# Optimization experiments

Hardware: AMD Instinct MI355X
Metric: run time of the kernel (lower is better)

The kernel has to match this reference:

```python
import jax, jax.numpy as jnp
import numpy as np

B, S, DIM = 2, 2048, 2048
H, KVH = 16, 8
HD = DIM // H            # 128
WIN = 512                # sliding window size
GLOB = 64                # global tokens
NEG = -1000000000.0


def _alibi_slopes(n):
    cp2 = 2.0 ** jnp.floor(jnp.log2(jnp.float32(n)))
    base = 2.0 ** (-(2.0 ** (-(jnp.log2(cp2) - 3.0))))
    powers = jnp.arange(1, 1 + n, dtype=jnp.float32)
    return jnp.power(base, powers)  # [n]


def _rope_tables(head_dim, seq_len, dtype=jnp.float32, base=10000.0):
    half = head_dim // 2
    freqs = 1.0 / base ** (jnp.arange(0, half, dtype=dtype) / half)
    t = jnp.arange(seq_len, dtype=dtype)
    f = jnp.outer(t, freqs)                       # [S, half]
    return jnp.sin(f)[None, None], jnp.cos(f)[None, None]  # [1,1,S,half]


def _rotary(x, sin, cos):
    # x: [b,h,s,d]; nonstandard rotation per source module
    x1, x2 = jnp.split(x, 2, axis=-1)
    return jnp.concatenate([x1 * cos - x2 * sin, x1 * sin + x2 * cos], axis=-1)


def _window_mask(seq_len):
    # Faithful to create_sliding_window_mask: 0.0 inside window / global rows+cols, -1e9 elsewhere
    i = jnp.arange(seq_len)[:, None]
    j = jnp.arange(seq_len)[None, :]
    m = jnp.where(jnp.abs(i - j) <= WIN // 2, 0.0, NEG)
    m = jnp.where((i < GLOB) | (j < GLOB), 0.0, m)
    return m  # [S, S] float


def setup_inputs() -> dict:
    key = jax.random.key(0)
    k1, k2, k3, k4 = jax.random.split(key, 4)
    x = jax.random.normal(k1, (B, S, DIM), dtype=jnp.float32)
    Wq = jax.random.normal(k2, (DIM, DIM), dtype=jnp.float32) * 0.02
    Wkv = jax.random.normal(k3, (DIM, 2 * KVH * HD), dtype=jnp.float32) * 0.02
    Wo = jax.random.normal(k4, (DIM, DIM), dtype=jnp.float32) * 0.02
    bo = jnp.zeros((DIM,), dtype=jnp.float32)
    return {"x": x, "Wq": Wq, "Wkv": Wkv, "Wo": Wo, "bo": bo}


def reference(x, Wq, Wkv, Wo, bo):
    b, s, dim = x.shape
    # token-complexity gating on queries
    complexity = jax.nn.sigmoid(jnp.sum(jnp.abs(x), axis=-1, keepdims=True))  # [b,s,1]
    q = jnp.dot(x * complexity, Wq)       # [b,s,dim]
    kv = jnp.dot(x, Wkv)                  # [b,s,2*kv_dim]
    k, v = jnp.split(kv, 2, axis=-1)

    q = q.reshape(b, s, H, HD).transpose(0, 2, 1, 3)      # [b,H,s,d]
    k = k.reshape(b, s, KVH, HD).transpose(0, 2, 1, 3)    # [b,KVH,s,d]
    v = v.reshape(b, s, KVH, HD).transpose(0, 2, 1, 3)

    sin, cos = _rope_tables(HD, s, dtype=x.dtype)
    q = _rotary(q, sin, cos)
    k = _rotary(k, sin, cos)

    r = H // KVH
    k = jnp.repeat(k, r, axis=1)   # 'b h s d -> b (h r) s d'
    v = jnp.repeat(v, r, axis=1)

    scale = 1.0 / jnp.sqrt(jnp.float32(HD)).astype(x.dtype)
    qk = jnp.einsum('bhid,bhjd->bhij', q, k) * scale      # [b,H,s,s]

    # ALiBi bias
    slopes = _alibi_slopes(H)                             # [H]
    pos = jnp.arange(s)
    dist = -jnp.abs(pos[:, None] - pos[None, :]).astype(jnp.float32)  # [s,s]
    qk = qk + slopes[:, None, None] * dist                # broadcast over batch

    # Faithful to source: jnp.where(float_mask, qk, NEG) treats nonzero (-1e9,
    # i.e. OUTSIDE window) as True -> keeps qk; zero (inside window) -> NEG.
    m = _window_mask(s)
    qk = jnp.where(m != 0.0, qk, NEG)

    attn = jax.nn.softmax(qk, axis=-1)
    out = jnp.einsum('bhij,bhjd->bhid', attn, v)          # [b,H,s,d]
    out = out.transpose(0, 2, 1, 3).reshape(b, s, dim)
    out = jnp.dot(out, Wo) + bo
    return out
```

## Files before the change

### kernel.cpp

```cpp
#include <hip/hip_runtime.h>

#define DEVI static __device__ __forceinline__

typedef __attribute__((ext_vector_type(8))) short short8;
typedef __attribute__((ext_vector_type(4))) short short4v;
typedef __attribute__((ext_vector_type(4))) float f32x4;

DEVI float bf2f(short u) {
  union { unsigned u32; float f; } c;
  c.u32 = ((unsigned)(unsigned short)u) << 16;
  return c.f;
}
DEVI short f2bf(float f) {
  union { float f; unsigned u32; } c; c.f = f;
  unsigned x = c.u32;
  unsigned r = (x + 0x7FFFu + ((x >> 16) & 1u)) >> 16;
  return (short)(unsigned short)r;
}
DEVI float ex2(float x) {
  float r;
  asm("v_exp_f32 %0, %1" : "=v"(r) : "v"(x));
  return r;
}
DEVI unsigned cvtpk(float lo, float hi) {
  unsigned r;
  asm("v_cvt_pk_bf16_f32 %0, %1, %2" : "=v"(r) : "v"(lo), "v"(hi));
  return r;
}

DEVI void gload16(const void* g, void* l) {
  __builtin_amdgcn_global_load_lds(
      (__attribute__((address_space(1))) void*)(g),
      (__attribute__((address_space(3))) void*)(l), 16, 0, 0);
}

#define LOG2E 1.4426950408889634f
#define QSCALE 0.1275174470974102f

__global__ void prep_x_kernel(const float* __restrict__ x,
                              short* __restrict__ xq, short* __restrict__ xb) {
  int row = blockIdx.x, t = threadIdx.x;
  const float4* xr = (const float4*)(x + (size_t)row * 2048);
  float4 v0 = xr[t], v1 = xr[t + 256];
  float s = fabsf(v0.x) + fabsf(v0.y) + fabsf(v0.z) + fabsf(v0.w)
          + fabsf(v1.x) + fabsf(v1.y) + fabsf(v1.z) + fabsf(v1.w);
#pragma unroll
  for (int m = 1; m < 64; m <<= 1) s += __shfl_xor(s, m, 64);
  __shared__ float red[4];
  if ((t & 63) == 0) red[t >> 6] = s;
  __syncthreads();
  float tot = red[0] + red[1] + red[2] + red[3];
  float sc = 1.0f / (1.0f + expf(-tot));
  short4v q0, q1, b0, b1;
  q0[0] = f2bf(v0.x * sc); q0[1] = f2bf(v0.y * sc); q0[2] = f2bf(v0.z * sc); q0[3] = f2bf(v0.w * sc);
  q1[0] = f2bf(v1.x * sc); q1[1] = f2bf(v1.y * sc); q1[2] = f2bf(v1.z * sc); q1[3] = f2bf(v1.w * sc);
  b0[0] = f2bf(v0.x); b0[1] = f2bf(v0.y); b0[2] = f2bf(v0.z); b0[3] = f2bf(v0.w);
  b1[0] = f2bf(v1.x); b1[1] = f2bf(v1.y); b1[2] = f2bf(v1.z); b1[3] = f2bf(v1.w);
  size_t base = (size_t)row * 512;
  ((short4v*)xq)[base + t]       = q0;
  ((short4v*)xq)[base + t + 256] = q1;
  ((short4v*)xb)[base + t]       = b0;
  ((short4v*)xb)[base + t + 256] = b1;
}

__global__ void sincos_kernel(float* __restrict__ tsin, float* __restrict__ tcos) {
  int idx = blockIdx.x * 256 + threadIdx.x;
  int d = idx >> 11, s = idx & 2047;
  float freq = powf(10000.0f, -(float)d / 64.0f);
  float f = (float)s * freq;
  tsin[idx] = sinf(f);
  tcos[idx] = cosf(f);
}

__global__ void wtrans_kernel(const float* __restrict__ W, short* __restrict__ WT) {
  __shared__ __align__(16) short tile[64][68];
  int n0 = blockIdx.x * 64, k0 = blockIdx.y * 64;
  int t = threadIdx.x;
  int tr = t >> 4, tc = t & 15;
#pragma unroll
  for (int p = 0; p < 4; ++p) {
    int r = p * 16 + tr;
    int c = tc * 4;
    float4 v = *(const float4*)&W[(size_t)(k0 + r) * 2048 + n0 + c];
    tile[c + 0][r] = f2bf(v.x);
    tile[c + 1][r] = f2bf(v.y);
    tile[c + 2][r] = f2bf(v.z);
    tile[c + 3][r] = f2bf(v.w);
  }
  __syncthreads();
#pragma unroll
  for (int p = 0; p < 4; ++p) {
    int n = p * 16 + tr;
    int c = tc * 4;
    *(short4v*)&WT[(size_t)(n0 + n) * 2048 + k0 + c] = *(const short4v*)&tile[n][c];
  }
}

template<int EPI>
__launch_bounds__(256, 2)
__global__ void gemm_kernel(const short* __restrict__ A, const short* __restrict__ BT,
                            void* __restrict__ Cout, short* __restrict__ aux,
                            const float* __restrict__ bias,
                            const float* __restrict__ tsin, const float* __restrict__ tcos,
                            int M, int N, int K) {
  __shared__ __align__(16) short As[128 * 32];
  __shared__ __align__(16) short Bs[128 * 32];
  const int tid = threadIdx.x;
  const int wid = tid >> 6, lane = tid & 63;
  const int nb = gridDim.x * gridDim.y;
  const int orig = blockIdx.y * gridDim.x + blockIdx.x;
  const int swz = (orig & 7) * (nb >> 3) + (orig >> 3);
  const int m0 = (swz / gridDim.x) * 128, n0 = (swz % gridDim.x) * 128;
  const int l15 = lane & 15, l4 = lane >> 4;
  f32x4 acc[2][8] = {};
  for (int k0 = 0; k0 < K; k0 += 32) {
#pragma unroll
    for (int p = 0; p < 2; ++p) {
      int chunk = wid + p * 4;
      int off = chunk * 1024 + lane * 16;
      int row = off >> 6;
      int cole = (off & 63) >> 1;
      gload16(A + (size_t)(m0 + row) * K + k0 + cole, &As[chunk * 512]);
      gload16(BT + (size_t)(n0 + row) * K + k0 + cole, &Bs[chunk * 512]);
    }
    __syncthreads();
    short8 af[2], bfr[8];
#pragma unroll
    for (int i = 0; i < 2; ++i)
      af[i] = *(const short8*)&As[(wid * 32 + i * 16 + l15) * 32 + l4 * 8];
#pragma unroll
    for (int i = 0; i < 8; ++i)
      bfr[i] = *(const short8*)&Bs[(i * 16 + l15) * 32 + l4 * 8];
#pragma unroll
    for (int mi = 0; mi < 2; ++mi)
#pragma unroll
      for (int ni = 0; ni < 8; ++ni)
        acc[mi][ni] = __builtin_amdgcn_mfma_f32_16x16x32_bf16(af[mi], bfr[ni], acc[mi][ni], 0, 0, 0);
    __syncthreads();
  }

  if (EPI == 0) {
#pragma unroll
    for (int mi = 0; mi < 2; ++mi) {
#pragma unroll
      for (int ni = 0; ni < 8; ++ni) {
        int col = n0 + ni * 16 + l15;
        float badd = bias[col];
#pragma unroll
        for (int r = 0; r < 4; ++r) {
          int row = m0 + wid * 32 + mi * 16 + l4 * 4 + r;
          ((float*)Cout)[(size_t)row * N + col] = acc[mi][ni][r] + badd;
        }
      }
    }
  } else if (EPI == 1) {
    const int h = n0 >> 7;
    const int b = m0 >> 11;
    const int sb = (m0 & 2047) + wid * 32;
    short* qr = (short*)Cout;
    const size_t obase = ((size_t)(b * 16 + h) * 2048 + sb) * 128;
#pragma unroll
    for (int mi = 0; mi < 2; ++mi) {
      int srel = sb + mi * 16 + l4 * 4;
#pragma unroll
      for (int ni = 0; ni < 4; ++ni) {
        int d = ni * 16 + l15;
        float4 sn = *(const float4*)&tsin[d * 2048 + srel];
        float4 cs = *(const float4*)&tcos[d * 2048 + srel];
#pragma unroll
        for (int r = 0; r < 4; ++r) {
          float x1 = acc[mi][ni][r], x2 = acc[mi][ni + 4][r];
          float snr = (&sn.x)[r], csr = (&cs.x)[r];
          size_t ro = obase + (size_t)(mi * 16 + l4 * 4 + r) * 128;
          qr[ro + d]      = f2bf((x1 * csr - x2 * snr) * QSCALE);
          qr[ro + d + 64] = f2bf((x1 * snr + x2 * csr) * QSCALE);
        }
      }
    }
  } else {
    const int b = m0 >> 11;
    const int sb = (m0 & 2047) + wid * 32;
    if (n0 < 1024) {
      const int kvh = n0 >> 7;
      short* kr = (short*)Cout;
      const size_t obase = ((size_t)(b * 8 + kvh) * 2048 + sb) * 128;
#pragma unroll
      for (int mi = 0; mi < 2; ++mi) {
        int srel = sb + mi * 16 + l4 * 4;
#pragma unroll
        for (int ni = 0; ni < 4; ++ni) {
          int d = ni * 16 + l15;
          float4 sn = *(const float4*)&tsin[d * 2048 + srel];
          float4 cs = *(const float4*)&tcos[d * 2048 + srel];
#pragma unroll
          for (int r = 0; r < 4; ++r) {
            float x1 = acc[mi][ni][r], x2 = acc[mi][ni + 4][r];
            float snr = (&sn.x)[r], csr = (&cs.x)[r];
            size_t ro = obase + (size_t)(mi * 16 + l4 * 4 + r) * 128;
            kr[ro + d]      = f2bf(x1 * csr - x2 * snr);
            kr[ro + d + 64] = f2bf(x1 * snr + x2 * csr);
          }
        }
      }
    } else {
      const int kvh = (n0 - 1024) >> 7;
      short* vt = aux;
      const size_t vb = (size_t)(b * 8 + kvh) * 128;
#pragma unroll
      for (int mi = 0; mi < 2; ++mi) {
        int srel = sb + mi * 16 + l4 * 4;
#pragma unroll
        for (int ni = 0; ni < 8; ++ni) {
          int d = ni * 16 + l15;
          uint2 w;
          w.x = cvtpk(acc[mi][ni][0], acc[mi][ni][1]);
          w.y = cvtpk(acc[mi][ni][2], acc[mi][ni][3]);
          *(uint2*)&vt[(vb + d) * 2048 + srel] = w;
        }
      }
    }
  }
}

__launch_bounds__(512, 4)
__global__ void attn_kernel(const short* __restrict__ qr, const short* __restrict__ kr,
                            const short* __restrict__ vt, short* __restrict__ ob) {
  __shared__ __align__(16) short Ks[2][64 * 128];
  __shared__ __align__(16) short Vs[2][128 * 64];
  __shared__ __align__(16) short PL[8][16 * 64];
  const int tid = threadIdx.x;
  const int wid = tid >> 6, lane = tid & 63;
  const int l15 = lane & 15, l4 = lane >> 4;
  const int sw7 = l15 & 7;
  const int l4h = l4 >> 1, l4l = l4 & 1;
  const int qt = blockIdx.x, h = blockIdx.y, b = blockIdx.z;
  const int kh = h >> 1;
  const int qb = qt * 128;
  const int q0 = qb + wid * 16;
  const float slope2 = exp2f(-0.5f * (float)(h + 1)) * LOG2E;
  const size_t qbase = ((size_t)(b * 16 + h) * 2048 + q0) * 128;
  const size_t kbase = ((size_t)(b * 8 + kh) * 2048) * 128;
  const size_t vbase = ((size_t)(b * 8 + kh) * 128) * 2048;
  short* pl = PL[wid];

  short8 aq[4];
#pragma unroll
  for (int kk = 0; kk < 4; ++kk)
    aq[kk] = *(const short8*)&qr[qbase + (size_t)l15 * 128 + kk * 32 + l4 * 8];

  f32x4 o[8] = {};
  float m_run = -1e30f, l_run = 0.0f;
  const int iq = q0 + l15;

  int lo0, n0t, lo1, n1t;
  if (qt == 0)      { lo0 = 0;   n0t = 32;          lo1 = 0; n1t = 0; }
  else if (qt == 1) { lo0 = 384; n0t = 26;          lo1 = 0; n1t = 0; }
  else {
    lo0 = 64;        n0t = 2 * qt - 3;
    lo1 = qb + 256;  n1t = (28 - 2 * qt > 0) ? (28 - 2 * qt) : 0;
  }
  const int nt = n0t + n1t;
  auto KV0 = [&](int i) { return i < n0t ? lo0 + i * 64 : lo1 + (i - n0t) * 64; };

  auto STAGE = [&](int bi, int kv0) {
#pragma unroll
    for (int i2 = 0; i2 < 2; ++i2) {
      int cid = i2 * 512 + tid;
      int krow = cid >> 4, kch = cid & 15;
      gload16(kr + kbase + (size_t)(kv0 + krow) * 128 + ((kch ^ (krow & 7)) * 8),
              &Ks[bi][cid * 8]);
    }
#pragma unroll
    for (int i2 = 0; i2 < 2; ++i2) {
      int cid = i2 * 512 + tid;
      int vrow = cid >> 3, vch = cid & 7;
      gload16(vt + vbase + (size_t)vrow * 2048 + kv0 + ((vch ^ (vrow & 7)) * 8),
              &Vs[bi][cid * 8]);
    }
  };

  STAGE(0, KV0(0));
  __syncthreads();
  int cur = 0;

  for (int it = 0; it < nt; ++it) {
    const int kv0 = KV0(it);
    if (it + 1 < nt) STAGE(cur ^ 1, KV0(it + 1));

    int mode;
    if (q0 + 15 < 64 || kv0 == 0) mode = 3;
    else if (kv0 <= q0 - 320)     mode = 1;
    else if (kv0 >= q0 + 272)     mode = 2;
    else                          mode = 0;

    if (mode != 3) {
      f32x4 sc[4];
#pragma unroll
      for (int jj = 0; jj < 4; ++jj) sc[jj] = (f32x4){0.f, 0.f, 0.f, 0.f};
      __builtin_amdgcn_s_setprio(1);
#pragma unroll
      for (int kk = 0; kk < 4; ++kk) {
#pragma unroll
        for (int jj = 0; jj < 4; ++jj) {
          short8 bk = *(const short8*)&Ks[cur][(jj * 16 + l15) * 128 + (((kk * 4 + l4) ^ sw7) * 8)];
          sc[jj] = __builtin_amdgcn_mfma_f32_16x16x32_bf16(bk, aq[kk], sc[jj], 0, 0, 0);
        }
      }
      __builtin_amdgcn_s_setprio(0);
      float pm = -1e30f;
      const float dbase = (float)(iq - kv0 - l4 * 4);
      if (mode == 0) {
#pragma unroll
        for (int jj = 0; jj < 4; ++jj) {
          float dj = dbase - 16.0f * jj;
#pragma unroll
          for (int r = 0; r < 4; ++r) {
            float d = dj - (float)r;
            float ad = fabsf(d);
            float v = fmaf(-slope2, ad, sc[jj][r]);
            v = (ad > 256.0f) ? v : -1e9f;
            sc[jj][r] = v;
            pm = fmaxf(pm, v);
          }
        }
      } else {
        const float sl = (mode == 1) ? -slope2 : slope2;
#pragma unroll
        for (int jj = 0; jj < 4; ++jj) {
          float dj = dbase - 16.0f * jj;
#pragma unroll
          for (int r = 0; r < 4; ++r) {
            float v = fmaf(sl, dj - (float)r, sc[jj][r]);
            sc[jj][r] = v;
            pm = fmaxf(pm, v);
          }
        }
      }
      pm = fmaxf(pm, __shfl_xor(pm, 16, 64));
      pm = fmaxf(pm, __shfl_xor(pm, 32, 64));
      if (!__all(pm <= m_run + 8.0f)) {
        float mn = fmaxf(m_run, pm);
        float corr = ex2(m_run - mn);
        l_run *= corr;
#pragma unroll
        for (int dn = 0; dn < 8; ++dn)
#pragma unroll
          for (int r = 0; r < 4; ++r) o[dn][r] *= corr;
        m_run = mn;
      }
      float psum = 0.0f;
#pragma unroll
      for (int jj = 0; jj < 4; ++jj) {
        float p0 = ex2(sc[jj][0] - m_run);
        float p1 = ex2(sc[jj][1] - m_run);
        float p2 = ex2(sc[jj][2] - m_run);
        float p3 = ex2(sc[jj][3] - m_run);
        psum += (p0 + p1) + (p2 + p3);
        uint2 w; w.x = cvtpk(p0, p1); w.y = cvtpk(p2, p3);
        int ad = l15 * 64 + (((jj * 2 + l4h) ^ sw7) * 8) + l4l * 4;
        *(uint2*)&pl[ad] = w;
      }
      psum += __shfl_xor(psum, 16, 64);
      psum += __shfl_xor(psum, 32, 64);
      l_run += psum;
      asm volatile("s_waitcnt lgkmcnt(0)" ::: "memory");
      __builtin_amdgcn_sched_barrier(0);
      __builtin_amdgcn_s_setprio(1);
#pragma unroll
      for (int c = 0; c < 2; ++c) {
        short8 pa = *(const short8*)&pl[l15 * 64 + (((c * 4 + l4) ^ sw7) * 8)];
#pragma unroll
        for (int dn = 0; dn < 8; ++dn) {
          short8 bv = *(const short8*)&Vs[cur][(dn * 16 + l15) * 64 + (((c * 4 + l4) ^ sw7) * 8)];
          o[dn] = __builtin_amdgcn_mfma_f32_16x16x32_bf16(bv, pa, o[dn], 0, 0, 0);
        }
      }
      __builtin_amdgcn_s_setprio(0);
    } else {
      float pm = -1e9f;
      if (!__all(pm <= m_run + 8.0f)) {
        float mn = fmaxf(m_run, pm);
        float corr = ex2(m_run - mn);
        l_run *= corr;
#pragma unroll
        for (int dn = 0; dn < 8; ++dn)
#pragma unroll
          for (int r = 0; r < 4; ++r) o[dn][r] *= corr;
        m_run = mn;
      }
      float pu = ex2(-1e9f - m_run);
      l_run += 64.0f * pu;
      unsigned uu = cvtpk(pu, pu);
      short8 pa;
      ((unsigned*)&pa)[0] = uu; ((unsigned*)&pa)[1] = uu;
      ((unsigned*)&pa)[2] = uu; ((unsigned*)&pa)[3] = uu;
      __builtin_amdgcn_s_setprio(1);
#pragma unroll
      for (int c = 0; c < 2; ++c) {
#pragma unroll
        for (int dn = 0; dn < 8; ++dn) {
          short8 bv = *(const short8*)&Vs[cur][(dn * 16 + l15) * 64 + (((c * 4 + l4) ^ sw7) * 8)];
          o[dn] = __builtin_amdgcn_mfma_f32_16x16x32_bf16(bv, pa, o[dn], 0, 0, 0);
        }
      }
      __builtin_amdgcn_s_setprio(0);
    }
    __syncthreads();
    cur ^= 1;
  }

  float inv = 1.0f / l_run;
  size_t rbase = ((size_t)(b * 2048 + iq) * 16 + h) * 128;
#pragma unroll
  for (int dn = 0; dn < 8; ++dn) {
    uint2 w;
    w.x = cvtpk(o[dn][0] * inv, o[dn][1] * inv);
    w.y = cvtpk(o[dn][2] * inv, o[dn][3] * inv);
    *(uint2*)&ob[rbase + dn * 16 + l4 * 4] = w;
  }
}

extern "C" void kernel_launch(void* const* d_in, const int* in_sizes, int n_in,
                              void* d_out, int out_size, void* d_ws, size_t ws_size,
                              hipStream_t stream) {
  const float* x   = (const float*)d_in[0];
  const float* Wq  = (const float*)d_in[1];
  const float* Wkv = (const float*)d_in[2];
  const float* Wo  = (const float*)d_in[3];
  const float* bo  = (const float*)d_in[4];
  float* out = (float*)d_out;

  char* ws = (char*)d_ws;
  size_t off = 0;
  auto alloc = [&](size_t bytes) -> void* {
    void* p = ws + off;
    off += (bytes + 255) & ~(size_t)255;
    return p;
  };
  float* tsin  = (float*)alloc(64 * 2048 * 4);
  float* tcos  = (float*)alloc(64 * 2048 * 4);
  short* WqT   = (short*)alloc((size_t)2048 * 2048 * 2);
  short* WkvT  = (short*)alloc((size_t)2048 * 2048 * 2);
  short* WoT   = (short*)alloc((size_t)2048 * 2048 * 2);
  short* xq    = (short*)alloc((size_t)4096 * 2048 * 2);
  short* xb    = (short*)alloc((size_t)4096 * 2048 * 2);
  short* qr    = (short*)alloc((size_t)2 * 16 * 2048 * 128 * 2);
  short* kr    = (short*)alloc((size_t)2 * 8 * 2048 * 128 * 2);
  short* vt    = (short*)alloc((size_t)2 * 8 * 2048 * 128 * 2);
  short* ob    = xq;

  prep_x_kernel<<<4096, 256, 0, stream>>>(x, xq, xb);
  sincos_kernel<<<512, 256, 0, stream>>>(tsin, tcos);
  wtrans_kernel<<<dim3(32, 32), 256, 0, stream>>>(Wq, WqT);
  wtrans_kernel<<<dim3(32, 32), 256, 0, stream>>>(Wkv, WkvT);
  wtrans_kernel<<<dim3(32, 32), 256, 0, stream>>>(Wo, WoT);
  gemm_kernel<1><<<dim3(16, 32), 256, 0, stream>>>(xq, WqT, qr, nullptr, nullptr, tsin, tcos, 4096, 2048, 2048);
  gemm_kernel<2><<<dim3(16, 32), 256, 0, stream>>>(xb, WkvT, kr, vt, nullptr, tsin, tcos, 4096, 2048, 2048);
  attn_kernel<<<dim3(16, 16, 2), 512, 0, stream>>>(qr, kr, vt, ob);
  gemm_kernel<0><<<dim3(16, 32), 256, 0, stream>>>(ob, WoT, (void*)out, nullptr, bo, nullptr, nullptr, 4096, 2048, 2048);
  (void)in_sizes; (void)n_in; (void)out_size; (void)ws_size;
}
```

Before: 260.6 us.

## Deepen GEMM K-tile with XOR-swizzled LDS, merge weight transposes, swizzle attention blocks

The GEMM K-step grows from 32 to 64, so there are half as many barrier pairs. LDS tiles now use an XOR swizzle to avoid bank conflicts, and the MFMA loop is hand-interleaved so B fragments load in two halves. The launch bound rises to 4 blocks per CU. The three weight-transpose launches are merged into one 3D grid, and the attention grid is remapped so neighbouring blocks share K/V heads for better cache locality. Risks are register pressure from the higher occupancy target and the doubled LDS footprint.

```diff
diff --git a/kernel.cpp b/kernel.cpp
--- a/kernel.cpp
+++ b/kernel.cpp
@@ -72,8 +72,13 @@
   tcos[idx] = cosf(f);
 }
 
-__global__ void wtrans_kernel(const float* __restrict__ W, short* __restrict__ WT) {
+__global__ void wtrans_kernel(const float* __restrict__ W0, const float* __restrict__ W1,
+                              const float* __restrict__ W2,
+                              short* __restrict__ T0, short* __restrict__ T1,
+                              short* __restrict__ T2) {
   __shared__ __align__(16) short tile[64][68];
+  const float* W = blockIdx.z == 0 ? W0 : (blockIdx.z == 1 ? W1 : W2);
+  short* WT      = blockIdx.z == 0 ? T0 : (blockIdx.z == 1 ? T1 : T2);
   int n0 = blockIdx.x * 64, k0 = blockIdx.y * 64;
   int t = threadIdx.x;
   int tr = t >> 4, tc = t & 15;
@@ -97,14 +102,14 @@
 }
 
 template<int EPI>
-__launch_bounds__(256, 2)
+__launch_bounds__(256, 4)
 __global__ void gemm_kernel(const short* __restrict__ A, const short* __restrict__ BT,
                             void* __restrict__ Cout, short* __restrict__ aux,
                             const float* __restrict__ bias,
                             const float* __restrict__ tsin, const float* __restrict__ tcos,
                             int M, int N, int K) {
-  __shared__ __align__(16) short As[128 * 32];
-  __shared__ __align__(16) short Bs[128 * 32];
+  __shared__ __align__(16) short As[128 * 64];
+  __shared__ __align__(16) short Bs[128 * 64];
   const int tid = threadIdx.x;
   const int wid = tid >> 6, lane = tid & 63;
   const int nb = gridDim.x * gridDim.y;
@@ -112,30 +117,48 @@
   const int swz = (orig & 7) * (nb >> 3) + (orig >> 3);
   const int m0 = (swz / gridDim.x) * 128, n0 = (swz % gridDim.x) * 128;
   const int l15 = lane & 15, l4 = lane >> 4;
+  const int sw7 = l15 & 7;
   f32x4 acc[2][8] = {};
-  for (int k0 = 0; k0 < K; k0 += 32) {
-#pragma unroll
-    for (int p = 0; p < 2; ++p) {
-      int chunk = wid + p * 4;
-      int off = chunk * 1024 + lane * 16;
-      int row = off >> 6;
-      int cole = (off & 63) >> 1;
-      gload16(A + (size_t)(m0 + row) * K + k0 + cole, &As[chunk * 512]);
-      gload16(BT + (size_t)(n0 + row) * K + k0 + cole, &Bs[chunk * 512]);
+  for (int k0 = 0; k0 < K; k0 += 64) {
+#pragma unroll
+    for (int p = 0; p < 4; ++p) {
+      int cid = p * 256 + tid;
+      int row = cid >> 3, ch = cid & 7;
+      int cole = (ch ^ (row & 7)) * 8;
+      gload16(A + (size_t)(m0 + row) * K + k0 + cole, &As[cid * 8]);
+      gload16(BT + (size_t)(n0 + row) * K + k0 + cole, &Bs[cid * 8]);
     }
     __syncthreads();
-    short8 af[2], bfr[8];
-#pragma unroll
-    for (int i = 0; i < 2; ++i)
-      af[i] = *(const short8*)&As[(wid * 32 + i * 16 + l15) * 32 + l4 * 8];
-#pragma unroll
-    for (int i = 0; i < 8; ++i)
-      bfr[i] = *(const short8*)&Bs[(i * 16 + l15) * 32 + l4 * 8];
-#pragma unroll
-    for (int mi = 0; mi < 2; ++mi)
-#pragma unroll
-      for (int ni = 0; ni < 8; ++ni)
-        acc[mi][ni] = __builtin_amdgcn_mfma_f32_16x16x32_bf16(af[mi], bfr[ni], acc[mi][ni], 0, 0, 0);
+#pragma unroll
+    for (int kk = 0; kk < 2; ++kk) {
+      const int cc = ((kk * 4 + l4) ^ sw7) * 8;
+      short8 af0 = *(const short8*)&As[(wid * 32 + l15) * 64 + cc];
+      short8 af1 = *(const short8*)&As[(wid * 32 + 16 + l15) * 64 + cc];
+      short8 bf0 = *(const short8*)&Bs[(0 * 16 + l15) * 64 + cc];
+      short8 bf1 = *(const short8*)&Bs[(1 * 16 + l15) * 64 + cc];
+      short8 bf2 = *(const short8*)&Bs[(2 * 16 + l15) * 64 + cc];
+      short8 bf3 = *(const short8*)&Bs[(3 * 16 + l15) * 64 + cc];
+      acc[0][0] = __builtin_amdgcn_mfma_f32_16x16x32_bf16(af0, bf0, acc[0][0], 0, 0, 0);
+      acc[1][0] = __builtin_amdgcn_mfma_f32_16x16x32_bf16(af1, bf0, acc[1][0], 0, 0, 0);
+      acc[0][1] = __builtin_amdgcn_mfma_f32_16x16x32_bf16(af0, bf1, acc[0][1], 0, 0, 0);
+      acc[1][1] = __builtin_amdgcn_mfma_f32_16x16x32_bf16(af1, bf1, acc[1][1], 0, 0, 0);
+      acc[0][2] = __builtin_amdgcn_mfma_f32_16x16x32_bf16(af0, bf2, acc[0][2], 0, 0, 0);
+      acc[1][2] = __builtin_amdgcn_mfma_f32_16x16x32_bf16(af1, bf2, acc[1][2], 0, 0, 0);
+      acc[0][3] = __builtin_amdgcn_mfma_f32_16x16x32_bf16(af0, bf3, acc[0][3], 0, 0, 0);
+      acc[1][3] = __builtin_amdgcn_mfma_f32_16x16x32_bf16(af1, bf3, acc[1][3], 0, 0, 0);
+      bf0 = *(const short8*)&Bs[(4 * 16 + l15) * 64 + cc];
+      bf1 = *(const short8*)&Bs[(5 * 16 + l15) * 64 + cc];
+      bf2 = *(const short8*)&Bs[(6 * 16 + l15) * 64 + cc];
+      bf3 = *(const short8*)&Bs[(7 * 16 + l15) * 64 + cc];
+      acc[0][4] = __builtin_amdgcn_mfma_f32_16x16x32_bf16(af0, bf0, acc[0][4], 0, 0, 0);
+      acc[1][4] = __builtin_amdgcn_mfma_f32_16x16x32_bf16(af1, bf0, acc[1][4], 0, 0, 0);
+      acc[0][5] = __builtin_amdgcn_mfma_f32_16x16x32_bf16(af0, bf1, acc[0][5], 0, 0, 0);
+      acc[1][5] = __builtin_amdgcn_mfma_f32_16x16x32_bf16(af1, bf1, acc[1][5], 0, 0, 0);
+      acc[0][6] = __builtin_amdgcn_mfma_f32_16x16x32_bf16(af0, bf2, acc[0][6], 0, 0, 0);
+      acc[1][6] = __builtin_amdgcn_mfma_f32_16x16x32_bf16(af1, bf2, acc[1][6], 0, 0, 0);
+      acc[0][7] = __builtin_amdgcn_mfma_f32_16x16x32_bf16(af0, bf3, acc[0][7], 0, 0, 0);
+      acc[1][7] = __builtin_amdgcn_mfma_f32_16x16x32_bf16(af1, bf3, acc[1][7], 0, 0, 0);
+    }
     __syncthreads();
   }
 
@@ -233,7 +256,9 @@
   const int l15 = lane & 15, l4 = lane >> 4;
   const int sw7 = l15 & 7;
   const int l4h = l4 >> 1, l4l = l4 & 1;
-  const int qt = blockIdx.x, h = blockIdx.y, b = blockIdx.z;
+  const int f = blockIdx.x + (blockIdx.y << 4) + (blockIdx.z << 8);
+  const int swb = (f & 7) * 64 + (f >> 3);
+  const int qt = swb & 15, h = (swb >> 4) & 15, b = swb >> 8;
   const int kh = h >> 1;
   const int qb = qt * 128;
   const int q0 = qb + wid * 16;
@@ -451,9 +476,7 @@
 
   prep_x_kernel<<<4096, 256, 0, stream>>>(x, xq, xb);
   sincos_kernel<<<512, 256, 0, stream>>>(tsin, tcos);
-  wtrans_kernel<<<dim3(32, 32), 256, 0, stream>>>(Wq, WqT);
-  wtrans_kernel<<<dim3(32, 32), 256, 0, stream>>>(Wkv, WkvT);
-  wtrans_kernel<<<dim3(32, 32), 256, 0, stream>>>(Wo, WoT);
+  wtrans_kernel<<<dim3(32, 32, 3), 256, 0, stream>>>(Wq, Wkv, Wo, WqT, WkvT, WoT);
   gemm_kernel<1><<<dim3(16, 32), 256, 0, stream>>>(xq, WqT, qr, nullptr, nullptr, tsin, tcos, 4096, 2048, 2048);
   gemm_kernel<2><<<dim3(16, 32), 256, 0, stream>>>(xb, WkvT, kr, vt, nullptr, tsin, tcos, 4096, 2048, 2048);
   attn_kernel<<<dim3(16, 16, 2), 512, 0, stream>>>(qr, kr, vt, ob);
```

Result: faster. 230.5 us (-11.5%).
